# Kernel tuning notes

Hardware: AMD Instinct MI355X
Metric: run time of the kernel (lower is better)

Reference implementation:

```python
import jax, jax.numpy as jnp
import numpy as np

D_MODEL = 1024
NHEAD = 16
HEAD_DIM = D_MODEL // NHEAD
LN_EPS = 1e-5
ROPE_BASE = 10000.0


def _rope_cos_sin(n, head_dim):
    inv_freq = 1.0 / (ROPE_BASE ** (jnp.arange(0, head_dim, 2, dtype=jnp.float32) / head_dim))
    t = jnp.arange(n, dtype=jnp.float32)
    freqs = jnp.outer(t, inv_freq)  # (N, head_dim//2)
    return jnp.cos(freqs), jnp.sin(freqs)


def _apply_rope(x, cos, sin):
    # x: (B, H, N, hd); cos/sin: (N, hd//2)
    B, H, N, hd = x.shape
    xr = x.reshape(B, H, N, hd // 2, 2)
    x0, x1 = xr[..., 0], xr[..., 1]
    c = cos[None, None]
    s = sin[None, None]
    rot = jnp.stack([x0 * c - x1 * s, x0 * s + x1 * c], axis=-1)
    return rot.reshape(B, H, N, hd)


def setup_inputs() -> dict:
    key = jax.random.key(0)
    ks = jax.random.split(key, 6)
    D = D_MODEL
    scale = 1.0 / np.sqrt(D)
    x = jax.random.normal(ks[0], (2, 2048, D), dtype=jnp.float32)
    Wq = jax.random.normal(ks[1], (D, D), dtype=jnp.float32) * scale
    Wk = jax.random.normal(ks[2], (D, D), dtype=jnp.float32) * scale
    Wv = jax.random.normal(ks[3], (D, D), dtype=jnp.float32) * scale
    Wo = jax.random.normal(ks[4], (D, D), dtype=jnp.float32) * scale
    bq = jnp.zeros((D,), jnp.float32)
    bk = jnp.zeros((D,), jnp.float32)
    bv = jnp.zeros((D,), jnp.float32)
    bo = jnp.zeros((D,), jnp.float32)
    ln_w = jnp.ones((D,), jnp.float32)
    ln_b = jnp.zeros((D,), jnp.float32)
    return {"x": x, "ln_w": ln_w, "ln_b": ln_b, "Wq": Wq, "bq": bq,
            "Wk": Wk, "bk": bk, "Wv": Wv, "bv": bv, "Wo": Wo, "bo": bo}


def reference(x, ln_w, ln_b, Wq, bq, Wk, bk, Wv, bv, Wo, bo):
    B, N, D = x.shape
    H, hd = NHEAD, HEAD_DIM
    # LayerNorm
    mu = jnp.mean(x, axis=-1, keepdims=True)
    var = jnp.mean(jnp.square(x - mu), axis=-1, keepdims=True)
    xn = (x - mu) * jax.lax.rsqrt(var + LN_EPS) * ln_w + ln_b
    # QKV projections -> (B, H, N, hd)
    def proj(W, b):
        return (xn @ W.T + b).reshape(B, N, H, hd).transpose(0, 2, 1, 3)
    q = proj(Wq, bq)
    k = proj(Wk, bk)
    v = proj(Wv, bv)
    cos, sin = _rope_cos_sin(N, hd)
    q = _apply_rope(q, cos, sin)
    k = _apply_rope(k, cos, sin)
    scores = jnp.einsum('bhqd,bhkd->bhqk', q, k) / jnp.sqrt(jnp.float32(hd))
    attn = jax.nn.softmax(scores, axis=-1)
    out = jnp.einsum('bhqk,bhkd->bhqd', attn, v)
    out = out.transpose(0, 2, 1, 3).reshape(B, N, D)
    return x + out @ Wo.T + bo
```

## Files before the change

### kernel.cpp

```cpp
#include <hip/hip_runtime.h>


#define SEQ 2048
#define LN_EPS 1e-5f

using short8 = __attribute__((ext_vector_type(8))) short;
using f32x4  = __attribute__((ext_vector_type(4))) float;
using f32x16 = __attribute__((ext_vector_type(16))) float;

__device__ __forceinline__ unsigned short f2bf(float f) {
  union { float f; unsigned u; } v; v.f = f;
  unsigned r = v.u + 0x7FFFu + ((v.u >> 16) & 1u);
  return (unsigned short)(r >> 16);
}

__device__ __forceinline__ void async16(const void* g, void* l) {
  __builtin_amdgcn_global_load_lds(
      (const __attribute__((address_space(1))) void*)g,
      (__attribute__((address_space(3))) void*)l, 16, 0, 0);
}

__global__ __launch_bounds__(256) void prep_kernel(
    const float* __restrict__ x, const float* __restrict__ lnw, const float* __restrict__ lnb,
    const float* __restrict__ wq, const float* __restrict__ wk,
    const float* __restrict__ wv, const float* __restrict__ wo,
    unsigned short* __restrict__ wqkv, unsigned short* __restrict__ wob,
    unsigned short* __restrict__ xn, float2* __restrict__ tab) {
  const int b = blockIdx.x, t = threadIdx.x;
  if (b < 4096) {
    const int gid = b * 256 + t;
    const int m = gid >> 18, e4 = gid & 262143;
    const float* src = (m == 0) ? wq : (m == 1) ? wk : (m == 2) ? wv : wo;
    const float4 v = ((const float4*)src)[e4];
    ushort4 o; o.x = f2bf(v.x); o.y = f2bf(v.y); o.z = f2bf(v.z); o.w = f2bf(v.w);
    if (m < 3) ((ushort4*)wqkv)[(size_t)m * 262144 + e4] = o;
    else       ((ushort4*)wob)[e4] = o;
  } else if (b < 8192) {
    const int row = b - 4096;
    const float4 v = ((const float4*)(x + (size_t)row * 1024))[t];
    float s  = v.x + v.y + v.z + v.w;
    float s2 = v.x * v.x + v.y * v.y + v.z * v.z + v.w * v.w;
#pragma unroll
    for (int off = 32; off >= 1; off >>= 1) {
      s  += __shfl_xor(s, off);
      s2 += __shfl_xor(s2, off);
    }
    __shared__ float red[8];
    const int lane = t & 63, wave = t >> 6;
    if (lane == 0) { red[wave] = s; red[4 + wave] = s2; }
    __syncthreads();
    s  = red[0] + red[1] + red[2] + red[3];
    s2 = red[4] + red[5] + red[6] + red[7];
    const float mu   = s * (1.0f / 1024.0f);
    const float var  = s2 * (1.0f / 1024.0f) - mu * mu;
    const float rstd = rsqrtf(var + LN_EPS);
    const float4 wv4 = ((const float4*)lnw)[t];
    const float4 bv4 = ((const float4*)lnb)[t];
    ushort4 o;
    o.x = f2bf((v.x - mu) * rstd * wv4.x + bv4.x);
    o.y = f2bf((v.y - mu) * rstd * wv4.y + bv4.y);
    o.z = f2bf((v.z - mu) * rstd * wv4.z + bv4.z);
    o.w = f2bf((v.w - mu) * rstd * wv4.w + bv4.w);
    ((ushort4*)xn)[(size_t)row * 256 + t] = o;
  } else {
    const int gid = (b - 8192) * 256 + t;
    const int pos = gid >> 5, ip = gid & 31;
    const float invf = exp2f((float)ip * -0.4152410118609203f);
    const float fr = (float)pos * invf;
    tab[gid] = make_float2(cosf(fr), sinf(fr));
  }
}

__global__ __launch_bounds__(256, 3) void gemm_qkv_kernel(
    const unsigned short* __restrict__ A,
    const unsigned short* __restrict__ Bw,
    const float* __restrict__ bq, const float* __restrict__ bk, const float* __restrict__ bv,
    const float2* __restrict__ tab,
    unsigned short* __restrict__ qb, unsigned short* __restrict__ kbg,
    unsigned short* __restrict__ vtb) {
  __shared__ unsigned short lA[128 * 64];
  __shared__ unsigned short lB[128 * 64];
  const int tid = threadIdx.x;
  const int lane = tid & 63, wave = tid >> 6;
  const int lr = lane & 15, quad = lane >> 4;
  const int wm = (wave >> 1) * 64, wn = (wave & 1) * 64;
  const int n0 = blockIdx.x * 128, m0 = blockIdx.y * 128;
  const int r7 = lr & 7;
  const int lrow = lane >> 3, lcg = (lane & 7) ^ lrow;
  const int lin = blockIdx.y * gridDim.x + blockIdx.x;
  const int phase = ((lin >> 8) * 5) & 15;

  f32x4 acc[4][4];
#pragma unroll
  for (int i = 0; i < 4; ++i)
#pragma unroll
    for (int j = 0; j < 4; ++j) acc[i][j] = (f32x4){0.f, 0.f, 0.f, 0.f};

  for (int kt = 0; kt < 16; ++kt) {
    const int kofs = ((kt + phase) & 15) * 64;
    __syncthreads();
#pragma unroll
    for (int c = 0; c < 4; ++c) {
      const int chunk = wave * 4 + c;
      const int grow = chunk * 8 + lrow;
      async16(&A[(size_t)(m0 + grow) * 1024 + kofs + lcg * 8], &lA[chunk * 512]);
      async16(&Bw[(size_t)(n0 + grow) * 1024 + kofs + lcg * 8], &lB[chunk * 512]);
    }
    __syncthreads();
#pragma unroll
    for (int kk = 0; kk < 2; ++kk) {
      short8 a[4], b[4];
#pragma unroll
      for (int i = 0; i < 4; ++i)
        a[i] = *(const short8*)&lA[(wm + i * 16 + lr) * 64 + ((kk * 4 + quad) ^ r7) * 8];
#pragma unroll
      for (int j = 0; j < 4; ++j)
        b[j] = *(const short8*)&lB[(wn + j * 16 + lr) * 64 + ((kk * 4 + quad) ^ r7) * 8];
#pragma unroll
      for (int i = 0; i < 4; ++i)
#pragma unroll
        for (int j = 0; j < 4; ++j)
          acc[i][j] = __builtin_amdgcn_mfma_f32_16x16x32_bf16(a[i], b[j], acc[i][j], 0, 0, 0);
    }
  }

  const int which = n0 >> 10;
  const float* bias = (which == 0) ? bq : (which == 1) ? bk : bv;
  const float qs = (which == 0) ? 0.18033688011112042f : 1.0f;
#pragma unroll
  for (int i = 0; i < 4; ++i)
#pragma unroll
    for (int j = 0; j < 4; ++j)
#pragma unroll
      for (int r = 0; r < 4; ++r) {
        const int row = m0 + wm + i * 16 + quad * 4 + r;
        const int col = n0 + wn + j * 16 + lr;
        const int c = col & 1023;
        float val = (acc[i][j][r] + bias[c]) * qs;
        const int head = c >> 6, hd_i = c & 63;
        const int b_ = row >> 11, pos = row & 2047;
        if (which < 2) {
          const float partner = __shfl_xor(val, 1);
          const float2 cs = tab[(pos << 5) + (hd_i >> 1)];
          val = val * cs.x + partner * ((lane & 1) ? cs.y : -cs.y);
        }
        if (which == 2) {
          vtb[((size_t)((b_ * 16 + head) * 64 + hd_i)) * SEQ + pos] = f2bf(val);
        } else {
          const size_t didx = ((size_t)((b_ * 16 + head) * SEQ + pos)) * 64 + hd_i;
          if (which == 0) qb[didx] = f2bf(val);
          else            kbg[didx] = f2bf(val);
        }
      }
}

__global__ __launch_bounds__(256, 3) void gemm_o_kernel(
    const unsigned short* __restrict__ A,
    const unsigned short* __restrict__ Bw,
    const float* __restrict__ bo, const float* __restrict__ xres, float* __restrict__ out) {
  __shared__ unsigned short lA[128 * 64];
  __shared__ unsigned short lB[64 * 64];
  const int tid = threadIdx.x;
  const int lane = tid & 63, wave = tid >> 6;
  const int lr = lane & 15, quad = lane >> 4;
  const int wm = (wave >> 1) * 64, wn = (wave & 1) * 32;
  const int n0 = blockIdx.x * 64, m0 = blockIdx.y * 128;
  const int r7 = lr & 7;
  const int lrow = lane >> 3, lcg = (lane & 7) ^ lrow;
  const int lin = blockIdx.y * gridDim.x + blockIdx.x;
  const int phase = ((lin >> 8) * 8) & 15;

  f32x4 acc[4][2];
#pragma unroll
  for (int i = 0; i < 4; ++i)
#pragma unroll
    for (int j = 0; j < 2; ++j) acc[i][j] = (f32x4){0.f, 0.f, 0.f, 0.f};

  for (int kt = 0; kt < 16; ++kt) {
    const int kofs = ((kt + phase) & 15) * 64;
    __syncthreads();
#pragma unroll
    for (int c = 0; c < 4; ++c) {
      const int chunk = wave * 4 + c;
      const int grow = chunk * 8 + lrow;
      async16(&A[(size_t)(m0 + grow) * 1024 + kofs + lcg * 8], &lA[chunk * 512]);
    }
#pragma unroll
    for (int c = 0; c < 2; ++c) {
      const int chunk = wave * 2 + c;
      const int grow = chunk * 8 + lrow;
      async16(&Bw[(size_t)(n0 + grow) * 1024 + kofs + lcg * 8], &lB[chunk * 512]);
    }
    __syncthreads();
#pragma unroll
    for (int kk = 0; kk < 2; ++kk) {
      short8 a[4], b[2];
#pragma unroll
      for (int i = 0; i < 4; ++i)
        a[i] = *(const short8*)&lA[(wm + i * 16 + lr) * 64 + ((kk * 4 + quad) ^ r7) * 8];
#pragma unroll
      for (int j = 0; j < 2; ++j)
        b[j] = *(const short8*)&lB[(wn + j * 16 + lr) * 64 + ((kk * 4 + quad) ^ r7) * 8];
#pragma unroll
      for (int i = 0; i < 4; ++i)
#pragma unroll
        for (int j = 0; j < 2; ++j)
          acc[i][j] = __builtin_amdgcn_mfma_f32_16x16x32_bf16(a[i], b[j], acc[i][j], 0, 0, 0);
    }
  }

#pragma unroll
  for (int i = 0; i < 4; ++i)
#pragma unroll
    for (int j = 0; j < 2; ++j)
#pragma unroll
      for (int r = 0; r < 4; ++r) {
        const int row = m0 + wm + i * 16 + quad * 4 + r;
        const int col = n0 + wn + j * 16 + lr;
        const size_t idx = (size_t)row * 1024 + col;
        out[idx] = acc[i][j][r] + bo[col] + xres[idx];
      }
}

__global__ __launch_bounds__(512, 4) void attn_kernel(
    const unsigned short* __restrict__ qg, const unsigned short* __restrict__ kg,
    const unsigned short* __restrict__ vtg, unsigned short* __restrict__ ao) {
  __shared__ unsigned short lKf[2][2][4096];
  __shared__ unsigned short lVf[2][2][4096];
  const int tid = threadIdx.x;
  const int lane = tid & 63, w = tid >> 6;
  const int ws = w & 3, kh = w >> 2;
  const int l31 = lane & 31, hb = lane >> 5;
  const int bh = blockIdx.x >> 4, qt = blockIdx.x & 15;
  const int q0w = qt * 128 + ws * 32;
  const int phase = ((blockIdx.x >> 8) * 8) & 15;
  const unsigned short* Q  = qg + (size_t)bh * SEQ * 64;
  const unsigned short* K  = kg + (size_t)bh * SEQ * 64;
  const unsigned short* VT = vtg + (size_t)bh * 64 * SEQ;

  short8 qf[4];
#pragma unroll
  for (int c = 0; c < 4; ++c)
    qf[c] = *(const short8*)&Q[(size_t)(q0w + l31) * 64 + c * 16 + hb * 8];

  f32x16 o[2];
#pragma unroll
  for (int dh = 0; dh < 2; ++dh)
#pragma unroll
    for (int r = 0; r < 16; ++r) o[dh][r] = 0.f;
  float ls = 0.f;

  const int srow = ws * 16 + (lane & 15);
  const int g0 = (lane >> 4) * 2;
  const int khbase = kh * 1024;
  const unsigned short* Ksrc = K + (size_t)(khbase + srow) * 64 + g0 * 8;
  const unsigned short* Vsrc = VT + (size_t)srow * SEQ + khbase + g0 * 8;
  const int kds0 = (((srow >> 5) * 8 + g0) * 32 + (srow & 31)) * 8;
  const int kds1 = kds0 + 256;
  const int vds0 = ((g0 * 2 + (srow >> 5)) * 32 + (srow & 31)) * 8;
  const int vds1 = vds0 + 512;

  short8 R0, R1, R2, R3;
  {
    const int kb = phase;
    R0 = *(const short8*)(Ksrc + kb * 4096);
    R1 = *(const short8*)(Ksrc + kb * 4096 + 8);
    R2 = *(const short8*)(Vsrc + kb * 64);
    R3 = *(const short8*)(Vsrc + kb * 64 + 8);
    *(short8*)&lKf[0][kh][kds0] = R0;
    *(short8*)&lKf[0][kh][kds1] = R1;
    *(short8*)&lVf[0][kh][vds0] = R2;
    *(short8*)&lVf[0][kh][vds1] = R3;
  }
  __syncthreads();

  for (int kt = 0; kt < 16; ++kt) {
    const int cur = kt & 1;
    if (kt < 15) {
      const int kb = (kt + 1 + phase) & 15;
      R0 = *(const short8*)(Ksrc + kb * 4096);
      R1 = *(const short8*)(Ksrc + kb * 4096 + 8);
      R2 = *(const short8*)(Vsrc + kb * 64);
      R3 = *(const short8*)(Vsrc + kb * 64 + 8);
    }
    const unsigned short* Kb = &lKf[cur][kh][0];
    const unsigned short* Vb = &lVf[cur][kh][0];

#pragma unroll
    for (int kb2 = 0; kb2 < 2; ++kb2) {
      f32x16 sv;
#pragma unroll
      for (int r = 0; r < 16; ++r) sv[r] = 0.f;
#pragma unroll
      for (int c = 0; c < 4; ++c) {
        const short8 af = *(const short8*)&Kb[((kb2 * 8 + c * 2 + hb) * 32 + l31) * 8];
        sv = __builtin_amdgcn_mfma_f32_32x32x16_bf16(af, qf[c], sv, 0, 0, 0);
      }
      unsigned wp[8];
#pragma unroll
      for (int p = 0; p < 8; ++p) {
        union { float f; unsigned u; } e0, e1;
        e0.f = __builtin_amdgcn_exp2f(sv[2 * p]);
        e1.f = __builtin_amdgcn_exp2f(sv[2 * p + 1]);
        ls += e0.f + e1.f;
        wp[p] = __builtin_amdgcn_perm(e1.u, e0.u, 0x07060302u);
      }
      unsigned wlo[8], whi[8];
#pragma unroll
      for (int p = 0; p < 8; ++p) {
        auto rr = __builtin_amdgcn_permlane32_swap(wp[p], wp[p], false, false);
        wlo[p] = rr[0]; whi[p] = rr[1];
      }
#pragma unroll
      for (int cl = 0; cl < 2; ++cl) {
        const int pb = cl * 4;
        union { unsigned u[4]; short8 s; } pf;
        pf.u[0] = hb ? wlo[pb + 2] : wlo[pb + 0];
        pf.u[1] = hb ? wlo[pb + 3] : wlo[pb + 1];
        pf.u[2] = hb ? whi[pb + 2] : whi[pb + 0];
        pf.u[3] = hb ? whi[pb + 3] : whi[pb + 1];
        const int ch = kb2 * 2 + cl;
#pragma unroll
        for (int dh = 0; dh < 2; ++dh) {
          const short8 vf = *(const short8*)&Vb[(((ch * 2 + hb) * 2 + dh) * 32 + l31) * 8];
          o[dh] = __builtin_amdgcn_mfma_f32_32x32x16_bf16(pf.s, vf, o[dh], 0, 0, 0);
        }
      }
    }

    if (kt < 15) {
      *(short8*)&lKf[cur ^ 1][kh][kds0] = R0;
      *(short8*)&lKf[cur ^ 1][kh][kds1] = R1;
      *(short8*)&lVf[cur ^ 1][kh][vds0] = R2;
      *(short8*)&lVf[cur ^ 1][kh][vds1] = R3;
    }
    __syncthreads();
  }

  union { float f; unsigned u; } lsu; lsu.f = ls;
  auto lr2 = __builtin_amdgcn_permlane32_swap(lsu.u, lsu.u, false, false);
  union { unsigned u; float f; } la, lb2; la.u = lr2[0]; lb2.u = lr2[1];
  const float lsH = la.f + lb2.f;

  float* osh = (float*)&lKf[0][0][0];
  float* lsh = (float*)&lVf[0][0][0];
  if (kh == 1) {
#pragma unroll
    for (int dh = 0; dh < 2; ++dh)
#pragma unroll
      for (int r = 0; r < 16; ++r)
        osh[((ws * 2 + dh) * 16 + r) * 64 + lane] = o[dh][r];
    lsh[ws * 64 + lane] = lsH;
  }
  __syncthreads();
  if (kh == 0) {
    const float rl = 1.0f / (lsH + lsh[ws * 64 + lane]);
    const int b_ = bh >> 4, h = bh & 15;
#pragma unroll
    for (int r = 0; r < 16; ++r) {
      const int m = (r & 3) + 8 * (r >> 2) + 4 * hb;
      const float rlv = __shfl(rl, m);
      const int row = q0w + m;
#pragma unroll
      for (int dh = 0; dh < 2; ++dh) {
        const float ov = o[dh][r] + osh[((ws * 2 + dh) * 16 + r) * 64 + lane];
        ao[(size_t)(b_ * SEQ + row) * 1024 + h * 64 + dh * 32 + l31] = f2bf(ov * rlv);
      }
    }
  }
}

extern "C" void kernel_launch(void* const* d_in, const int* in_sizes, int n_in,
                              void* d_out, int out_size, void* d_ws, size_t ws_size,
                              hipStream_t stream) {
  const float* x   = (const float*)d_in[0];
  const float* lnw = (const float*)d_in[1];
  const float* lnb = (const float*)d_in[2];
  const float* Wq  = (const float*)d_in[3];
  const float* bq  = (const float*)d_in[4];
  const float* Wk  = (const float*)d_in[5];
  const float* bk  = (const float*)d_in[6];
  const float* Wv  = (const float*)d_in[7];
  const float* bv  = (const float*)d_in[8];
  const float* Wo  = (const float*)d_in[9];
  const float* bo  = (const float*)d_in[10];
  float* out = (float*)d_out;

  char* ws = (char*)d_ws;
  unsigned short* wqkv = (unsigned short*)(ws);
  unsigned short* wob  = (unsigned short*)(ws + 6291456);
  unsigned short* xn   = (unsigned short*)(ws + 8388608);
  unsigned short* qb   = (unsigned short*)(ws + 16777216);
  unsigned short* kbuf = (unsigned short*)(ws + 25165824);
  unsigned short* vtb  = (unsigned short*)(ws + 33554432);
  unsigned short* ao   = (unsigned short*)(ws + 41943040);
  float2*         tab  = (float2*)(ws + 50331648);

  hipLaunchKernelGGL(prep_kernel, dim3(8448), dim3(256), 0, stream,
                     x, lnw, lnb, Wq, Wk, Wv, Wo, wqkv, wob, xn, tab);
  hipLaunchKernelGGL(gemm_qkv_kernel, dim3(24, 32), dim3(256), 0, stream,
                     xn, wqkv, bq, bk, bv, tab, qb, kbuf, vtb);
  hipLaunchKernelGGL(attn_kernel, dim3(512), dim3(512), 0, stream, qb, kbuf, vtb, ao);
  hipLaunchKernelGGL(gemm_o_kernel, dim3(16, 32), dim3(256), 0, stream,
                     ao, wob, bo, x, out);
}
```

Baseline: 214.6 us.

## Restructure attention K/V staging into four 32-key slots with XOR-swizzled LDS

The attention kernel now stages K and V in four 32-key slots instead of two 64-key buffers. Each loop iteration processes two sub-tiles and holds only one block-wide barrier. The global loads for the next sub-tile are interleaved with compute on the current one. LDS addresses use an XOR swizzle to reduce bank conflicts, and s_setprio raises wave priority around the MFMA sections. LDS use stays at 64 KB, and register pressure may shift because the staging registers are reused twice per iteration.

```diff
diff --git a/kernel.cpp b/kernel.cpp
--- a/kernel.cpp
+++ b/kernel.cpp
@@ -225,15 +225,14 @@
 __global__ __launch_bounds__(512, 4) void attn_kernel(
     const unsigned short* __restrict__ qg, const unsigned short* __restrict__ kg,
     const unsigned short* __restrict__ vtg, unsigned short* __restrict__ ao) {
-  __shared__ unsigned short lKf[2][2][4096];
-  __shared__ unsigned short lVf[2][2][4096];
+  __shared__ unsigned short lds[32768];
   const int tid = threadIdx.x;
   const int lane = tid & 63, w = tid >> 6;
   const int ws = w & 3, kh = w >> 2;
   const int l31 = lane & 31, hb = lane >> 5;
   const int bh = blockIdx.x >> 4, qt = blockIdx.x & 15;
   const int q0w = qt * 128 + ws * 32;
-  const int phase = ((blockIdx.x >> 8) * 8) & 15;
+  const int phase32 = ((blockIdx.x >> 8) & 1) * 16;
   const unsigned short* Q  = qg + (size_t)bh * SEQ * 64;
   const unsigned short* K  = kg + (size_t)bh * SEQ * 64;
   const unsigned short* VT = vtg + (size_t)bh * 64 * SEQ;
@@ -250,89 +249,105 @@
     for (int r = 0; r < 16; ++r) o[dh][r] = 0.f;
   float ls = 0.f;
 
-  const int srow = ws * 16 + (lane & 15);
-  const int g0 = (lane >> 4) * 2;
   const int khbase = kh * 1024;
-  const unsigned short* Ksrc = K + (size_t)(khbase + srow) * 64 + g0 * 8;
-  const unsigned short* Vsrc = VT + (size_t)srow * SEQ + khbase + g0 * 8;
-  const int kds0 = (((srow >> 5) * 8 + g0) * 32 + (srow & 31)) * 8;
-  const int kds1 = kds0 + 256;
-  const int vds0 = ((g0 * 2 + (srow >> 5)) * 32 + (srow & 31)) * 8;
-  const int vds1 = vds0 + 512;
-
-  short8 R0, R1, R2, R3;
-  {
-    const int kb = phase;
-    R0 = *(const short8*)(Ksrc + kb * 4096);
-    R1 = *(const short8*)(Ksrc + kb * 4096 + 8);
-    R2 = *(const short8*)(Vsrc + kb * 64);
-    R3 = *(const short8*)(Vsrc + kb * 64 + 8);
-    *(short8*)&lKf[0][kh][kds0] = R0;
-    *(short8*)&lKf[0][kh][kds1] = R1;
-    *(short8*)&lVf[0][kh][vds0] = R2;
-    *(short8*)&lVf[0][kh][vds1] = R3;
+  const int srow_k = ws * 8 + (lane >> 3), gk = lane & 7;
+  const int srow_v = ws * 16 + (lane >> 2), gv = lane & 3;
+  const unsigned short* Ksrc = K + (size_t)(khbase + srow_k) * 64 + gk * 8;
+  const unsigned short* Vsrc = VT + (size_t)srow_v * SEQ + khbase + gv * 8;
+  const int kds = (gk * 32 + (srow_k ^ gk)) * 8;
+  const int g2s = gv * 2 + (srow_v >> 5);
+  const int vds = (g2s * 32 + ((srow_v & 31) ^ g2s)) * 8;
+  unsigned short* const base_kh = lds + kh * 4096;
+
+  int koff[4], voff[2][2];
+#pragma unroll
+  for (int c = 0; c < 4; ++c) {
+    const int fk = c * 2 + hb;
+    koff[c] = (fk * 32 + (l31 ^ fk)) * 8;
+  }
+#pragma unroll
+  for (int cl = 0; cl < 2; ++cl)
+#pragma unroll
+    for (int dh = 0; dh < 2; ++dh) {
+      const int f = (cl * 2 + hb) * 2 + dh;
+      voff[cl][dh] = 2048 + (f * 32 + (l31 ^ f)) * 8;
+    }
+
+  auto TILE = [&](const unsigned short* Tb) {
+    f32x16 sv;
+#pragma unroll
+    for (int r = 0; r < 16; ++r) sv[r] = 0.f;
+    __builtin_amdgcn_s_setprio(1);
+#pragma unroll
+    for (int c = 0; c < 4; ++c) {
+      const short8 af = *(const short8*)&Tb[koff[c]];
+      sv = __builtin_amdgcn_mfma_f32_32x32x16_bf16(af, qf[c], sv, 0, 0, 0);
+    }
+    __builtin_amdgcn_s_setprio(0);
+    unsigned wp[8];
+#pragma unroll
+    for (int p = 0; p < 8; ++p) {
+      union { float f; unsigned u; } e0, e1;
+      e0.f = __builtin_amdgcn_exp2f(sv[2 * p]);
+      e1.f = __builtin_amdgcn_exp2f(sv[2 * p + 1]);
+      ls += e0.f + e1.f;
+      wp[p] = __builtin_amdgcn_perm(e1.u, e0.u, 0x07060302u);
+    }
+    unsigned wlo[8], whi[8];
+#pragma unroll
+    for (int p = 0; p < 8; ++p) {
+      auto rr = __builtin_amdgcn_permlane32_swap(wp[p], wp[p], false, false);
+      wlo[p] = rr[0]; whi[p] = rr[1];
+    }
+    __builtin_amdgcn_s_setprio(1);
+#pragma unroll
+    for (int cl = 0; cl < 2; ++cl) {
+      const int pb = cl * 4;
+      union { unsigned u[4]; short8 s; } pf;
+      pf.u[0] = hb ? wlo[pb + 2] : wlo[pb + 0];
+      pf.u[1] = hb ? wlo[pb + 3] : wlo[pb + 1];
+      pf.u[2] = hb ? whi[pb + 2] : whi[pb + 0];
+      pf.u[3] = hb ? whi[pb + 3] : whi[pb + 1];
+#pragma unroll
+      for (int dh = 0; dh < 2; ++dh) {
+        const short8 vf = *(const short8*)&Tb[voff[cl][dh]];
+        o[dh] = __builtin_amdgcn_mfma_f32_32x32x16_bf16(pf.s, vf, o[dh], 0, 0, 0);
+      }
+    }
+    __builtin_amdgcn_s_setprio(0);
+  };
+
+#pragma unroll
+  for (int j = 0; j < 2; ++j) {
+    const int tl = (j + phase32) & 31;
+    const short8 R0 = *(const short8*)(Ksrc + (size_t)tl * 2048);
+    const short8 R2 = *(const short8*)(Vsrc + tl * 32);
+    *(short8*)(base_kh + j * 8192 + kds) = R0;
+    *(short8*)(base_kh + j * 8192 + 2048 + vds) = R2;
   }
   __syncthreads();
 
-  for (int kt = 0; kt < 16; ++kt) {
-    const int cur = kt & 1;
-    if (kt < 15) {
-      const int kb = (kt + 1 + phase) & 15;
-      R0 = *(const short8*)(Ksrc + kb * 4096);
-      R1 = *(const short8*)(Ksrc + kb * 4096 + 8);
-      R2 = *(const short8*)(Vsrc + kb * 64);
-      R3 = *(const short8*)(Vsrc + kb * 64 + 8);
-    }
-    const unsigned short* Kb = &lKf[cur][kh][0];
-    const unsigned short* Vb = &lVf[cur][kh][0];
-
-#pragma unroll
-    for (int kb2 = 0; kb2 < 2; ++kb2) {
-      f32x16 sv;
-#pragma unroll
-      for (int r = 0; r < 16; ++r) sv[r] = 0.f;
-#pragma unroll
-      for (int c = 0; c < 4; ++c) {
-        const short8 af = *(const short8*)&Kb[((kb2 * 8 + c * 2 + hb) * 32 + l31) * 8];
-        sv = __builtin_amdgcn_mfma_f32_32x32x16_bf16(af, qf[c], sv, 0, 0, 0);
-      }
-      unsigned wp[8];
-#pragma unroll
-      for (int p = 0; p < 8; ++p) {
-        union { float f; unsigned u; } e0, e1;
-        e0.f = __builtin_amdgcn_exp2f(sv[2 * p]);
-        e1.f = __builtin_amdgcn_exp2f(sv[2 * p + 1]);
-        ls += e0.f + e1.f;
-        wp[p] = __builtin_amdgcn_perm(e1.u, e0.u, 0x07060302u);
-      }
-      unsigned wlo[8], whi[8];
-#pragma unroll
-      for (int p = 0; p < 8; ++p) {
-        auto rr = __builtin_amdgcn_permlane32_swap(wp[p], wp[p], false, false);
-        wlo[p] = rr[0]; whi[p] = rr[1];
-      }
-#pragma unroll
-      for (int cl = 0; cl < 2; ++cl) {
-        const int pb = cl * 4;
-        union { unsigned u[4]; short8 s; } pf;
-        pf.u[0] = hb ? wlo[pb + 2] : wlo[pb + 0];
-        pf.u[1] = hb ? wlo[pb + 3] : wlo[pb + 1];
-        pf.u[2] = hb ? whi[pb + 2] : whi[pb + 0];
-        pf.u[3] = hb ? whi[pb + 3] : whi[pb + 1];
-        const int ch = kb2 * 2 + cl;
-#pragma unroll
-        for (int dh = 0; dh < 2; ++dh) {
-          const short8 vf = *(const short8*)&Vb[(((ch * 2 + hb) * 2 + dh) * 32 + l31) * 8];
-          o[dh] = __builtin_amdgcn_mfma_f32_32x32x16_bf16(pf.s, vf, o[dh], 0, 0, 0);
-        }
-      }
-    }
-
-    if (kt < 15) {
-      *(short8*)&lKf[cur ^ 1][kh][kds0] = R0;
-      *(short8*)&lKf[cur ^ 1][kh][kds1] = R1;
-      *(short8*)&lVf[cur ^ 1][kh][vds0] = R2;
-      *(short8*)&lVf[cur ^ 1][kh][vds1] = R3;
+  for (int it = 0; it < 16; ++it) {
+    const int cs = (it & 1) * 2;
+    const int ss = cs ^ 2;
+    short8 R0, R2;
+    if (it < 15) {
+      const int tl = (2 * it + 2 + phase32) & 31;
+      R0 = *(const short8*)(Ksrc + (size_t)tl * 2048);
+      R2 = *(const short8*)(Vsrc + tl * 32);
+    }
+    TILE(base_kh + cs * 8192);
+    if (it < 15) {
+      *(short8*)(base_kh + ss * 8192 + kds) = R0;
+      *(short8*)(base_kh + ss * 8192 + 2048 + vds) = R2;
+      const int tl = (2 * it + 3 + phase32) & 31;
+      R0 = *(const short8*)(Ksrc + (size_t)tl * 2048);
+      R2 = *(const short8*)(Vsrc + tl * 32);
+    }
+    TILE(base_kh + (cs + 1) * 8192);
+    if (it < 15) {
+      *(short8*)(base_kh + (ss + 1) * 8192 + kds) = R0;
+      *(short8*)(base_kh + (ss + 1) * 8192 + 2048 + vds) = R2;
     }
     __syncthreads();
   }
@@ -342,8 +357,8 @@
   union { unsigned u; float f; } la, lb2; la.u = lr2[0]; lb2.u = lr2[1];
   const float lsH = la.f + lb2.f;
 
-  float* osh = (float*)&lKf[0][0][0];
-  float* lsh = (float*)&lVf[0][0][0];
+  float* osh = (float*)lds;
+  float* lsh = (float*)(lds + 16384);
   if (kh == 1) {
 #pragma unroll
     for (int dh = 0; dh < 2; ++dh)
```

Result: faster. 207.2 us (-3.5%).
